# Optimization experiments

Hardware: AMD Instinct MI355X
Metric: run time of the kernel (lower is better)

Reference implementation:

```python
import jax, jax.numpy as jnp
import numpy as np
import math

B, L, D, H = 8, 1024, 64, 8   # batch, seq, d_model(=head_dim=d_k=d_v), heads
MAX_REL = 150

def _rel_idx(len_q, len_k):
    # [len_q, len_k] indices into (2*MAX_REL+1)-row table
    dist = jnp.arange(len_k)[None, :] - jnp.arange(len_q)[:, None]
    return jnp.clip(dist, -MAX_REL, MAX_REL) + MAX_REL

def setup_inputs() -> dict:
    key = jax.random.key(0)
    ks = jax.random.split(key, 9)
    def xavier(k, shape):
        fan_in, fan_out = shape[0], shape[1]
        bound = math.sqrt(6.0 / (fan_in + fan_out))
        return jax.random.uniform(k, shape, jnp.float32, -bound, bound)
    return {
        "query": jax.random.normal(ks[0], (B, L, D), jnp.float32),
        "key":   jax.random.normal(ks[1], (B, L, D), jnp.float32),
        "value": jax.random.normal(ks[2], (B, L, D), jnp.float32),
        # nn.Linear(d_model, H*D) stored here as [in, out] for x @ W
        "Wq": xavier(ks[3], (D, H * D)),
        "Wk": xavier(ks[4], (D, H * D)),
        "Wv": xavier(ks[5], (D, H * D)),
        "Wo": xavier(ks[6], (H * D, D)),
        "rel_k_table": xavier(ks[7], (2 * MAX_REL + 1, D)),
        "rel_v_table": xavier(ks[8], (2 * MAX_REL + 1, D)),
    }

def reference(query, key, value, Wq, Wk, Wv, Wo, rel_k_table, rel_v_table):
    b, lq, d = query.shape
    lk = key.shape[1]
    h = H
    scale = jnp.sqrt(jnp.asarray(d, query.dtype))  # sqrt(head_dim)=sqrt(d_model)

    q = (query @ Wq).reshape(b, lq, h, d)   # [b, lq, h, d]
    k = (key   @ Wk).reshape(b, lk, h, d)
    v = (value @ Wv).reshape(b, lk, h, d)

    # content-content scores
    attn1 = jnp.einsum('bqhd,bkhd->bhqk', q, k)
    # content-position scores: gather relative embeddings [lq, lk, d]
    idx = _rel_idx(lq, lk)
    rk = rel_k_table[idx]                    # [lq, lk, d]
    attn2 = jnp.einsum('bqhd,qkd->bhqk', q, rk)

    attn = jax.nn.softmax((attn1 + attn2) / scale, axis=-1)  # [b,h,lq,lk]

    weight1 = jnp.einsum('bhqk,bkhd->bhqd', attn, v)
    rv = rel_v_table[idx]                    # [lq, lk, d] (len_v == len_k)
    weight2 = jnp.einsum('bhqk,qkd->bhqd', attn, rv)

    x = (weight1 + weight2).transpose(0, 2, 1, 3).reshape(b, lq, h * d)
    return x @ Wo                            # [b, lq, d_model]
```

## Files before the change

### kernel.cpp

```cpp
#include <hip/hip_runtime.h>
#include <stdint.h>

#define B_   8
#define L_   1024
#define D_   64
#define H_   8
#define HD_  512
#define NREL 301
#define RP   320
#define RKB  304

#define QRSTR 312
#define PBSTR 328
#define PTSTR 72

typedef short bf16x8 __attribute__((ext_vector_type(8)));
typedef float f32x4  __attribute__((ext_vector_type(4)));

#define MFMA16(a,b,c) __builtin_amdgcn_mfma_f32_16x16x32_bf16((a),(b),(c),0,0,0)

__device__ __forceinline__ float bf2f(short s){
  union { unsigned u; float f; } v; v.u = ((unsigned)(unsigned short)s) << 16; return v.f;
}
__device__ __forceinline__ short f2bf(float f){
  union { float f; unsigned u; } v; v.f = f;
  v.u += ((v.u >> 16) & 1u) + 0x7fffu;
  return (short)(v.u >> 16);
}
__device__ __forceinline__ bf16x8 cvt8(const float* p){
  float4 x0 = *(const float4*)p, x1 = *(const float4*)(p + 4);
  bf16x8 r;
  r[0]=f2bf(x0.x); r[1]=f2bf(x0.y); r[2]=f2bf(x0.z); r[3]=f2bf(x0.w);
  r[4]=f2bf(x1.x); r[5]=f2bf(x1.y); r[6]=f2bf(x1.z); r[7]=f2bf(x1.w);
  return r;
}

#define PREP_TOTAL (4*32768 + 64*RP + RKB*64)
__global__ __launch_bounds__(256)
void prep_kernel(const float* __restrict__ Wq, const float* __restrict__ Wk,
                 const float* __restrict__ Wv, const float* __restrict__ Wo,
                 const float* __restrict__ rk, const float* __restrict__ rv,
                 short* __restrict__ ws16){
  int idx = blockIdx.x*256 + threadIdx.x;
  short* WqT = ws16;
  short* WkT = ws16 + 32768;
  short* WvT = ws16 + 65536;
  short* WoT = ws16 + 98304;
  short* rvT = ws16 + 131072;
  short* rkB = ws16 + 131072 + 64*RP;
  if (idx < 32768){ WqT[idx] = f2bf(Wq[(idx&63)*HD_ + (idx>>6)]); return; }
  idx -= 32768;
  if (idx < 32768){ WkT[idx] = f2bf(Wk[(idx&63)*HD_ + (idx>>6)]); return; }
  idx -= 32768;
  if (idx < 32768){ WvT[idx] = f2bf(Wv[(idx&63)*HD_ + (idx>>6)]); return; }
  idx -= 32768;
  if (idx < 32768){ WoT[idx] = f2bf(Wo[(idx&511)*D_ + (idx>>9)]); return; }
  idx -= 32768;
  if (idx < 64*RP){ int c = idx/RP, r = idx - c*RP;
                    rvT[idx] = (r < NREL) ? f2bf(rv[r*D_ + c]) : (short)0; return; }
  idx -= 64*RP;
  if (idx < RKB*64){ int tr = idx>>6, d = idx&63;
                     int src = (tr > 300) ? 300 : tr;
                     rkB[idx] = f2bf(rk[src*D_ + d]); }
}

__global__ __launch_bounds__(256)
void proj_kernel(const float* __restrict__ qin, const float* __restrict__ kin,
                 const float* __restrict__ vin,
                 const short* __restrict__ WqT, const short* __restrict__ WkT,
                 const short* __restrict__ WvT,
                 short* __restrict__ Qo, short* __restrict__ Ko, short* __restrict__ VTo){
  int t = threadIdx.x, w = t>>6, l = t&63;
  int mt = blockIdx.x, ny = blockIdx.y, mat = blockIdx.z;
  const float* in = (mat==0) ? qin : (mat==1 ? kin : vin);
  const short* WT = (mat==0) ? WqT : (mat==1 ? WkT : WvT);
  int arow = mt*64 + w*16 + (l&15);
  bf16x8 a[2];
#pragma unroll
  for (int kf=0;kf<2;++kf)
    a[kf] = cvt8(in + arow*D_ + (l>>4)*8 + kf*32);
  f32x4 acc[4];
#pragma unroll
  for (int nt=0;nt<4;++nt){
    f32x4 z = {0.f,0.f,0.f,0.f}; acc[nt] = z;
#pragma unroll
    for (int kf=0;kf<2;++kf){
      bf16x8 bfr = *(const bf16x8*)(WT + (ny*64 + nt*16 + (l&15))*D_ + (l>>4)*8 + kf*32);
      acc[nt] = MFMA16(a[kf], bfr, acc[nt]);
    }
  }
  float scale = (mat==0) ? 0.125f : 1.0f;
#pragma unroll
  for (int nt=0;nt<4;++nt){
    int hd = ny*64 + nt*16 + (l&15);
    int h = hd >> 6, d = hd & 63;
#pragma unroll
    for (int j=0;j<4;++j){
      int m = mt*64 + w*16 + (l>>4)*4 + j;
      int b = m >> 10, lr = m & 1023;
      short vv = f2bf(acc[nt][j] * scale);
      if (mat==2) VTo[(((b*H_ + h)*D_ + d)<<10) + lr] = vv;
      else {
        short* O = (mat==0) ? Qo : Ko;
        O[((((b*H_ + h)<<10) + lr)*D_) + d] = vv;
      }
    }
  }
}

__global__ __launch_bounds__(64)
void attn_kernel(const short* __restrict__ Q, const short* __restrict__ K,
                 const short* __restrict__ VT, const short* __restrict__ rkB,
                 const short* __restrict__ rvT, short* __restrict__ X){
  __shared__ short QRs[16*QRSTR];
  __shared__ short Pband[16*PBSTR];
  __shared__ short Pt[16*PTSTR];
  int l = threadIdx.x, g = l>>4, c = l&15;
  int qt = blockIdx.x, h = blockIdx.y, b = blockIdx.z;
  int q0 = qt*16;
  const short* Qg  = Q  + ((((b*H_ + h)<<10) + q0)*D_);
  const short* Kg  = K  + (((b*H_ + h)<<10)*D_);
  const short* VTg = VT + (((b*H_ + h)*D_)<<10);

  { uint4 z = {0,0,0,0};
#pragma unroll
    for (int i=0;i<11;++i){ int u = i*64 + l; if (u < 16*PBSTR/8) ((uint4*)Pband)[u] = z; } }

  bf16x8 aq[2];
#pragma unroll
  for (int kf=0;kf<2;++kf)
    aq[kf] = *(const bf16x8*)(Qg + c*D_ + g*8 + kf*32);

  for (int nt=0; nt<19; ++nt){
    f32x4 cf = {0.f,0.f,0.f,0.f};
    int r = nt*16 + c;
#pragma unroll
    for (int kf=0;kf<2;++kf)
      cf = MFMA16(aq[kf], *(const bf16x8*)(rkB + r*D_ + g*8 + kf*32), cf);
#pragma unroll
    for (int j=0;j<4;++j)
      QRs[(4*g + j)*QRSTR + r] = f2bf(cf[j]);
  }

  f32x4 av[4]; { f32x4 z = {0.f,0.f,0.f,0.f}; av[0]=z; av[1]=z; av[2]=z; av[3]=z; }
  float pj[4] = {0.f,0.f,0.f,0.f}, e0[4] = {0.f,0.f,0.f,0.f}, e1[4] = {0.f,0.f,0.f,0.f};

  bf16x8 kb[4][2], kn[4][2], vb[4][2];
#pragma unroll
  for (int nt=0;nt<4;++nt)
#pragma unroll
    for (int kf=0;kf<2;++kf)
      kb[nt][kf] = *(const bf16x8*)(Kg + (nt*16 + c)*D_ + g*8 + kf*32);

  for (int kt=0; kt<16; ++kt){
#pragma unroll
    for (int nt=0;nt<4;++nt)
#pragma unroll
      for (int kf=0;kf<2;++kf)
        vb[nt][kf] = *(const bf16x8*)(VTg + ((nt*16 + c)<<10) + kt*64 + g*8 + kf*32);
    int ktn = (kt < 15) ? kt+1 : 15;
#pragma unroll
    for (int nt=0;nt<4;++nt)
#pragma unroll
      for (int kf=0;kf<2;++kf)
        kn[nt][kf] = *(const bf16x8*)(Kg + (ktn*64 + nt*16 + c)*D_ + g*8 + kf*32);

    f32x4 s[4]; { f32x4 z = {0.f,0.f,0.f,0.f}; s[0]=z; s[1]=z; s[2]=z; s[3]=z; }
#pragma unroll
    for (int nt=0;nt<4;++nt)
#pragma unroll
      for (int kf=0;kf<2;++kf)
        s[nt] = MFMA16(aq[kf], kb[nt][kf], s[nt]);

#pragma unroll
    for (int nt=0;nt<4;++nt){
      int kg = kt*64 + nt*16 + c;
#pragma unroll
      for (int j=0;j<4;++j){
        int ql = 4*g + j;
        int dd = kg - (q0 + ql);
        int r  = (dd < -150 ? -150 : (dd > 150 ? 150 : dd)) + 150;
        float sv = s[nt][j] + bf2f(QRs[ql*QRSTR + r]);
        float p  = __expf(sv);
        pj[j] += p;
        short pb = f2bf(p);
        if (dd <= -150)      e0[j] += p;
        else if (dd >= 150)  e1[j] += p;
        else                 Pband[ql*PBSTR + dd + 150] = pb;
        Pt[ql*PTSTR + nt*16 + c] = pb;
      }
    }

#pragma unroll
    for (int kf=0;kf<2;++kf){
      bf16x8 pa = *(const bf16x8*)(Pt + c*PTSTR + g*8 + kf*32);
#pragma unroll
      for (int nt=0;nt<4;++nt)
        av[nt] = MFMA16(pa, vb[nt][kf], av[nt]);
    }
#pragma unroll
    for (int nt=0;nt<4;++nt)
#pragma unroll
      for (int kf=0;kf<2;++kf)
        kb[nt][kf] = kn[nt][kf];
  }

#pragma unroll
  for (int j=0;j<4;++j){
    float v = pj[j];
    v += __shfl_xor(v,1); v += __shfl_xor(v,2); v += __shfl_xor(v,4); v += __shfl_xor(v,8);
    pj[j] = v;
    float a0 = e0[j];
    a0 += __shfl_xor(a0,1); a0 += __shfl_xor(a0,2); a0 += __shfl_xor(a0,4); a0 += __shfl_xor(a0,8);
    e0[j] = a0;
    float a1 = e1[j];
    a1 += __shfl_xor(a1,1); a1 += __shfl_xor(a1,2); a1 += __shfl_xor(a1,4); a1 += __shfl_xor(a1,8);
    e1[j] = a1;
  }
  if (c == 0){
#pragma unroll
    for (int j=0;j<4;++j){
      Pband[(4*g + j)*PBSTR + 0]   = f2bf(e0[j]);
      Pband[(4*g + j)*PBSTR + 300] = f2bf(e1[j]);
    }
  }

#pragma unroll
  for (int kf=0; kf<10; ++kf){
    bf16x8 wa = *(const bf16x8*)(Pband + c*PBSTR + g*8 + kf*32);
#pragma unroll
    for (int nt=0;nt<4;++nt)
      av[nt] = MFMA16(wa, *(const bf16x8*)(rvT + (nt*16 + c)*RP + g*8 + kf*32), av[nt]);
  }

  float rl[4];
#pragma unroll
  for (int j=0;j<4;++j) rl[j] = 1.0f / pj[j];
#pragma unroll
  for (int nt=0;nt<4;++nt){
    int col = h*64 + nt*16 + c;
#pragma unroll
    for (int j=0;j<4;++j){
      int row = (b<<10) + q0 + 4*g + j;
      X[row*HD_ + col] = f2bf(av[nt][j] * rl[j]);
    }
  }
}

__global__ __launch_bounds__(64)
void out_kernel(const short* __restrict__ X, const short* __restrict__ WoT,
                float* __restrict__ out){
  int l = threadIdx.x, mt = blockIdx.x;
  f32x4 acc[4]; { f32x4 z = {0.f,0.f,0.f,0.f}; acc[0]=z; acc[1]=z; acc[2]=z; acc[3]=z; }
  const short* Xg = X + mt*16*HD_;
#pragma unroll
  for (int kf=0; kf<16; ++kf){
    bf16x8 a = *(const bf16x8*)(Xg + (l&15)*HD_ + (l>>4)*8 + kf*32);
#pragma unroll
    for (int nt=0;nt<4;++nt){
      bf16x8 bfr = *(const bf16x8*)(WoT + (nt*16 + (l&15))*HD_ + (l>>4)*8 + kf*32);
      acc[nt] = MFMA16(a, bfr, acc[nt]);
    }
  }
#pragma unroll
  for (int nt=0;nt<4;++nt)
#pragma unroll
    for (int j=0;j<4;++j)
      out[(mt*16 + (l>>4)*4 + j)*D_ + nt*16 + (l&15)] = acc[nt][j];
}

__global__ __launch_bounds__(256)
void zero_out_kernel(float* __restrict__ out, int n){
  int i = blockIdx.x*256 + threadIdx.x;
  if (i < n) out[i] = 0.f;
}

extern "C" void kernel_launch(void* const* d_in, const int* in_sizes, int n_in,
                              void* d_out, int out_size, void* d_ws, size_t ws_size,
                              hipStream_t stream){
  (void)in_sizes; (void)n_in;
  const float* q  = (const float*)d_in[0];
  const float* k  = (const float*)d_in[1];
  const float* v  = (const float*)d_in[2];
  const float* Wq = (const float*)d_in[3];
  const float* Wk = (const float*)d_in[4];
  const float* Wv = (const float*)d_in[5];
  const float* Wo = (const float*)d_in[6];
  const float* rk = (const float*)d_in[7];
  const float* rv = (const float*)d_in[8];

  const size_t NEED = 342016u + 4u*8388608u;
  if (ws_size < NEED){
    zero_out_kernel<<<(out_size + 255)/256, 256, 0, stream>>>((float*)d_out, out_size);
    return;
  }
  char* ws = (char*)d_ws;
  short* WqT = (short*)(ws);
  short* WkT = (short*)(ws + 65536);
  short* WvT = (short*)(ws + 131072);
  short* WoT = (short*)(ws + 196608);
  short* rvT = (short*)(ws + 262144);
  short* rkB = (short*)(ws + 303104);
  short* Q   = (short*)(ws + 342016);
  short* K   = (short*)(ws + 342016 + 8388608);
  short* VT  = (short*)(ws + 342016 + 2u*8388608);
  short* X   = (short*)(ws + 342016 + 3u*8388608);

  prep_kernel<<<(PREP_TOTAL + 255)/256, 256, 0, stream>>>(Wq, Wk, Wv, Wo, rk, rv, (short*)ws);
  proj_kernel<<<dim3(128, 8, 3), 256, 0, stream>>>(q, k, v, WqT, WkT, WvT, Q, K, VT);
  attn_kernel<<<dim3(64, 8, 8), 64, 0, stream>>>(Q, K, VT, rkB, rvT, X);
  out_kernel<<<512, 64, 0, stream>>>(X, WoT, (float*)d_out);
}
```

Before: 214.0 us.

## Software-pipeline QK scores one tile ahead and remap blocks per XCD

Restructures the attention loop so the QK^T MFMA for the next key tile is issued before the softmax and PV work of the current tile. K is prefetched two tiles ahead and V one tile ahead, using ping-pong register buffers in a 2x unrolled macro body. It also flattens the grid and remaps block indices so each XCD handles whole (batch, head) groups, which should improve L2 reuse of K/V. LDS strides shrink to 304/320, and the masked zero fill loop is simplified to match. The costs are extra register pressure from doubled K/V/score buffers and possible LDS bank conflicts from the new strides.

```diff
diff --git a/kernel.cpp b/kernel.cpp
--- a/kernel.cpp
+++ b/kernel.cpp
@@ -10,8 +10,8 @@
 #define RP   320
 #define RKB  304
 
-#define QRSTR 312
-#define PBSTR 328
+#define QRSTR 304
+#define PBSTR 320
 #define PTSTR 72
 
 typedef short bf16x8 __attribute__((ext_vector_type(8)));
@@ -116,15 +116,31 @@
   __shared__ short Pband[16*PBSTR];
   __shared__ short Pt[16*PTSTR];
   int l = threadIdx.x, g = l>>4, c = l&15;
-  int qt = blockIdx.x, h = blockIdx.y, b = blockIdx.z;
+  int n = blockIdx.x;
+  int xcd = n & 7, idx = n >> 3;
+  int bh = xcd * 8 + (idx >> 6);
+  int qt = idx & 63;
+  int b = bh >> 3, h = bh & 7;
   int q0 = qt*16;
   const short* Qg  = Q  + ((((b*H_ + h)<<10) + q0)*D_);
   const short* Kg  = K  + (((b*H_ + h)<<10)*D_);
   const short* VTg = VT + (((b*H_ + h)*D_)<<10);
 
+  bf16x8 kbA[4][2], kbB[4][2], vbA[4][2], vbB[4][2];
+  f32x4 sA[4], sB[4];
+
+#pragma unroll
+  for (int nt=0;nt<4;++nt)
+#pragma unroll
+    for (int kf=0;kf<2;++kf){
+      kbA[nt][kf] = *(const bf16x8*)(Kg + (nt*16 + c)*D_ + g*8 + kf*32);
+      kbB[nt][kf] = *(const bf16x8*)(Kg + (64 + nt*16 + c)*D_ + g*8 + kf*32);
+      vbA[nt][kf] = *(const bf16x8*)(VTg + ((nt*16 + c)<<10) + g*8 + kf*32);
+    }
+
   { uint4 z = {0,0,0,0};
 #pragma unroll
-    for (int i=0;i<11;++i){ int u = i*64 + l; if (u < 16*PBSTR/8) ((uint4*)Pband)[u] = z; } }
+    for (int i=0;i<10;++i) ((uint4*)Pband)[i*64 + l] = z; }
 
   bf16x8 aq[2];
 #pragma unroll
@@ -142,68 +158,67 @@
       QRs[(4*g + j)*QRSTR + r] = f2bf(cf[j]);
   }
 
+#pragma unroll
+  for (int nt=0;nt<4;++nt){ f32x4 z = {0.f,0.f,0.f,0.f}; sA[nt] = z; }
+#pragma unroll
+  for (int nt=0;nt<4;++nt)
+#pragma unroll
+    for (int kf=0;kf<2;++kf)
+      sA[nt] = MFMA16(aq[kf], kbA[nt][kf], sA[nt]);
+
   f32x4 av[4]; { f32x4 z = {0.f,0.f,0.f,0.f}; av[0]=z; av[1]=z; av[2]=z; av[3]=z; }
   float pj[4] = {0.f,0.f,0.f,0.f}, e0[4] = {0.f,0.f,0.f,0.f}, e1[4] = {0.f,0.f,0.f,0.f};
 
-  bf16x8 kb[4][2], kn[4][2], vb[4][2];
-#pragma unroll
-  for (int nt=0;nt<4;++nt)
-#pragma unroll
-    for (int kf=0;kf<2;++kf)
-      kb[nt][kf] = *(const bf16x8*)(Kg + (nt*16 + c)*D_ + g*8 + kf*32);
-
-  for (int kt=0; kt<16; ++kt){
-#pragma unroll
-    for (int nt=0;nt<4;++nt)
-#pragma unroll
-      for (int kf=0;kf<2;++kf)
-        vb[nt][kf] = *(const bf16x8*)(VTg + ((nt*16 + c)<<10) + kt*64 + g*8 + kf*32);
-    int ktn = (kt < 15) ? kt+1 : 15;
-#pragma unroll
-    for (int nt=0;nt<4;++nt)
-#pragma unroll
-      for (int kf=0;kf<2;++kf)
-        kn[nt][kf] = *(const bf16x8*)(Kg + (ktn*64 + nt*16 + c)*D_ + g*8 + kf*32);
-
-    f32x4 s[4]; { f32x4 z = {0.f,0.f,0.f,0.f}; s[0]=z; s[1]=z; s[2]=z; s[3]=z; }
-#pragma unroll
-    for (int nt=0;nt<4;++nt)
-#pragma unroll
-      for (int kf=0;kf<2;++kf)
-        s[nt] = MFMA16(aq[kf], kb[nt][kf], s[nt]);
-
-#pragma unroll
-    for (int nt=0;nt<4;++nt){
-      int kg = kt*64 + nt*16 + c;
-#pragma unroll
-      for (int j=0;j<4;++j){
-        int ql = 4*g + j;
-        int dd = kg - (q0 + ql);
-        int r  = (dd < -150 ? -150 : (dd > 150 ? 150 : dd)) + 150;
-        float sv = s[nt][j] + bf2f(QRs[ql*QRSTR + r]);
-        float p  = __expf(sv);
-        pj[j] += p;
-        short pb = f2bf(p);
-        if (dd <= -150)      e0[j] += p;
-        else if (dd >= 150)  e1[j] += p;
-        else                 Pband[ql*PBSTR + dd + 150] = pb;
-        Pt[ql*PTSTR + nt*16 + c] = pb;
-      }
-    }
-
-#pragma unroll
-    for (int kf=0;kf<2;++kf){
-      bf16x8 pa = *(const bf16x8*)(Pt + c*PTSTR + g*8 + kf*32);
-#pragma unroll
-      for (int nt=0;nt<4;++nt)
-        av[nt] = MFMA16(pa, vb[nt][kf], av[nt]);
-    }
-#pragma unroll
-    for (int nt=0;nt<4;++nt)
-#pragma unroll
-      for (int kf=0;kf<2;++kf)
-        kb[nt][kf] = kn[nt][kf];
-  }
+#define TILE_BODY(KT, kbC, kbN, vbC, vbN, sC, sN)                              \
+  {                                                                            \
+    int ktn = (KT)+2 < 16 ? (KT)+2 : 15;                                       \
+    int vtn = (KT)+1 < 16 ? (KT)+1 : 15;                                       \
+    _Pragma("unroll")                                                          \
+    for (int nt=0;nt<4;++nt)                                                   \
+      _Pragma("unroll")                                                        \
+      for (int kf=0;kf<2;++kf){                                                \
+        kbN[nt][kf] = *(const bf16x8*)(Kg + (ktn*64 + nt*16 + c)*D_ + g*8 + kf*32); \
+        vbN[nt][kf] = *(const bf16x8*)(VTg + ((nt*16 + c)<<10) + vtn*64 + g*8 + kf*32); \
+      }                                                                        \
+    _Pragma("unroll")                                                          \
+    for (int nt=0;nt<4;++nt){ f32x4 z = {0.f,0.f,0.f,0.f}; sN[nt] = z; }       \
+    _Pragma("unroll")                                                          \
+    for (int nt=0;nt<4;++nt)                                                   \
+      _Pragma("unroll")                                                        \
+      for (int kf=0;kf<2;++kf)                                                 \
+        sN[nt] = MFMA16(aq[kf], kbC[nt][kf], sN[nt]);                          \
+    _Pragma("unroll")                                                          \
+    for (int nt=0;nt<4;++nt){                                                  \
+      int kg = (KT)*64 + nt*16 + c;                                            \
+      _Pragma("unroll")                                                        \
+      for (int j=0;j<4;++j){                                                   \
+        int ql = 4*g + j;                                                      \
+        int dd = kg - (q0 + ql);                                               \
+        int r  = (dd < -150 ? -150 : (dd > 150 ? 150 : dd)) + 150;             \
+        float sv = sC[nt][j] + bf2f(QRs[ql*QRSTR + r]);                        \
+        float p  = __expf(sv);                                                 \
+        pj[j] += p;                                                            \
+        short pb = f2bf(p);                                                    \
+        if (dd <= -150)      e0[j] += p;                                       \
+        else if (dd >= 150)  e1[j] += p;                                       \
+        else                 Pband[ql*PBSTR + dd + 150] = pb;                  \
+        Pt[ql*PTSTR + nt*16 + c] = pb;                                         \
+      }                                                                        \
+    }                                                                          \
+    _Pragma("unroll")                                                          \
+    for (int kf=0;kf<2;++kf){                                                  \
+      bf16x8 pa = *(const bf16x8*)(Pt + c*PTSTR + g*8 + kf*32);                \
+      _Pragma("unroll")                                                        \
+      for (int nt=0;nt<4;++nt)                                                 \
+        av[nt] = MFMA16(pa, vbC[nt][kf], av[nt]);                              \
+    }                                                                          \
+  }
+
+  for (int kt = 0; kt < 16; kt += 2){
+    TILE_BODY(kt,   kbB, kbA, vbA, vbB, sA, sB);
+    TILE_BODY(kt+1, kbA, kbB, vbB, vbA, sB, sA);
+  }
+#undef TILE_BODY
 
 #pragma unroll
   for (int j=0;j<4;++j){
@@ -308,6 +323,6 @@
 
   prep_kernel<<<(PREP_TOTAL + 255)/256, 256, 0, stream>>>(Wq, Wk, Wv, Wo, rk, rv, (short*)ws);
   proj_kernel<<<dim3(128, 8, 3), 256, 0, stream>>>(q, k, v, WqT, WkT, WvT, Q, K, VT);
-  attn_kernel<<<dim3(64, 8, 8), 64, 0, stream>>>(Q, K, VT, rkB, rvT, X);
+  attn_kernel<<<4096, 64, 0, stream>>>(Q, K, VT, rkB, rvT, X);
   out_kernel<<<512, 64, 0, stream>>>(X, WoT, (float*)d_out);
 }
```

Result: slower. 224.4 us (+4.8%).
